# Performance work log

Measured on AMD Instinct MI355X. Metric: run time of the kernel, lower is better.

## Reference

```python
import jax, jax.numpy as jnp
import numpy as np

B, K, D, H, A = 8192, 10, 64, 128, 16
E = K * (K - 1)
# lexicographic ordered pairs (i,j), i != j -- matches adj.nonzero() and sorted(Dict.keys())
_PAIRS = np.array([(i, j) for i in range(K) for j in range(K) if i != j], dtype=np.int32)
SRC = jnp.asarray(_PAIRS[:, 0])  # message for edge (i,j) is aggregated at node i (row)
DST = jnp.asarray(_PAIRS[:, 1])


def setup_inputs() -> dict:
    key = jax.random.key(0)
    k1, k2, k3, k4, k5, k6 = jax.random.split(key, 6)
    F = D + H + A  # node MLP input dim
    return {
        "states": jax.random.normal(k1, (B, K, D), jnp.float32),
        "action_vec": jax.random.normal(k2, (B, K, A), jnp.float32),
        # one Linear(2D -> H) per ordered pair, stacked [E, 2D, H]
        "W_edge": jax.random.normal(k3, (E, 2 * D, H), jnp.float32) * (1.0 / np.sqrt(2 * D)),
        "b_edge": jax.random.normal(k4, (E, H), jnp.float32) * 0.01,
        # one Linear(D+H+A -> D) per node, stacked [K, F, D]
        "W_node": jax.random.normal(k5, (K, F, D), jnp.float32) * (1.0 / np.sqrt(F)),
        "b_node": jax.random.normal(k6, (K, D), jnp.float32) * 0.01,
    }


def reference(states, action_vec, W_edge, b_edge, W_node, b_node):
    # states: [B,K,D], action_vec: [B,K,A]
    b, k, d = states.shape
    # gather endpoints per ordered edge: [B,E,2D]
    pair_feat = jnp.concatenate([states[:, SRC, :], states[:, DST, :]], axis=-1)
    # per-edge-type Linear + tanh, batched as one grouped GEMM: [B,E,H]
    msg = jnp.tanh(jnp.einsum('bef,efh->beh', pair_feat, W_edge) + b_edge)
    # unsorted_segment_sum over source node index (row): [B,K,H]
    agg = jnp.zeros((b, k, msg.shape[-1]), msg.dtype).at[:, SRC, :].add(msg)
    # node input: [x, action, agg] -> per-node Linear + tanh: [B,K,D]
    node_in = jnp.concatenate([states, action_vec, agg], axis=-1)
    out = jnp.tanh(jnp.einsum('bkf,kfd->bkd', node_in, W_node) + b_node)
    return out
```

## Files before the change

### kernel.cpp

```cpp
#include <hip/hip_runtime.h>

typedef _Float16 f16;
typedef _Float16 f16x4 __attribute__((ext_vector_type(4)));
typedef _Float16 f16x8 __attribute__((ext_vector_type(8)));
typedef float    f32x4 __attribute__((ext_vector_type(4)));

#define S2C 2.88539008177792681472f

#define OFF_STF  0u
#define OFF_AC   5242880u
#define OFF_WEF  6553600u
#define OFF_WNF  8028160u
#define OFF_BE2  8171520u
#define OFF_Z    8195840u

__device__ __forceinline__ float fast_exp2(float x){
#if __has_builtin(__builtin_amdgcn_exp2f)
    return __builtin_amdgcn_exp2f(x);
#else
    return exp2f(x);
#endif
}
__device__ __forceinline__ float fast_rcp(float x){
#if __has_builtin(__builtin_amdgcn_rcpf)
    return __builtin_amdgcn_rcpf(x);
#else
    return 1.0f/x;
#endif
}

#define MFMA16(a,b,c) __builtin_amdgcn_mfma_f32_16x16x32_f16(a,b,c,0,0,0)

__global__ void prep(const float* __restrict__ st, const float* __restrict__ ac,
                     const float* __restrict__ We, const float* __restrict__ be,
                     const float* __restrict__ Wn, const float* __restrict__ bn,
                     f16* __restrict__ ws16){
    const int bid = blockIdx.x, t = threadIdx.x;
    if (bid < 2560){
        int g = bid*256 + t;
        int lane = g&63, ks = (g>>6)&1, rt = (g>>7)&1, rg2 = (g>>8)&255, node = g>>16;
        int row = rg2*32 + rt*16 + (lane&15);
        int k   = ks*32 + (lane>>4)*8;
        const float* src = st + ((size_t)row*10 + node)*64 + k;
        const float4 v0 = *(const float4*)src;
        const float4 v1 = *(const float4*)(src+4);
        f16x8 h; h[0]=(f16)v0.x; h[1]=(f16)v0.y; h[2]=(f16)v0.z; h[3]=(f16)v0.w;
                 h[4]=(f16)v1.x; h[5]=(f16)v1.y; h[6]=(f16)v1.z; h[7]=(f16)v1.w;
        *(f16x8*)(ws16 + OFF_STF + (size_t)g*8) = h;
    } else if (bid < 3840){
        int g = (bid-2560)*256 + t;
        const float4 v = ((const float4*)ac)[g];
        f16x4 h; h[0]=(f16)v.x; h[1]=(f16)v.y; h[2]=(f16)v.z; h[3]=(f16)v.w;
        *(f16x4*)(ws16 + OFF_AC + (size_t)g*4) = h;
    } else if (bid < 4560){
        int g = (bid-3840)*256 + t;
        int l = g & 15, q = (g>>4)&3, cg = (g>>6)&7, ks = (g>>9)&3, e = g>>11;
        const float* src = We + e*16384 + (ks*32 + q*8)*128 + cg*16 + l;
        f16x8 h;
        #pragma unroll
        for (int u=0;u<8;u++) h[u] = (f16)src[u*128];
        *(f16x8*)(ws16 + OFF_WEF + (size_t)g*8) = h;
    } else if (bid < 4630){
        int g = (bid-4560)*256 + t;
        if (g < 17920){
            int l = g&15, q=(g>>4)&3, c=(g>>6)&3, r=g>>8;
            int ks2 = r % 7, kn = r / 7;
            f16x8 h;
            #pragma unroll
            for (int u=0;u<8;u++){
                int knew = ks2*32 + q*8 + u;
                int f = (knew < 128) ? (knew + 80) : (knew - 128);
                h[u] = (knew < 208) ? (f16)Wn[kn*13312 + f*64 + c*16 + l] : (f16)0.0f;
            }
            *(f16x8*)(ws16 + OFF_WNF + (size_t)kn*14336 + ((size_t)(ks2*4+c)*64 + q*16 + l)*8) = h;
        }
    } else {
        int g = (bid-4630)*256 + t;
        float* be2 = (float*)(ws16 + OFF_BE2);
        if (g < 11520)      be2[g] = S2C*be[g];
        else if (g < 12160) be2[g] = S2C*bn[g-11520];
        else if (g < 12168) ws16[OFF_Z + (g-12160)] = (f16)0.0f;
    }
}

__launch_bounds__(256, 3)
__global__ void gnn_main(const f16* __restrict__ ws16, float* __restrict__ out){
    __shared__ alignas(16) f16 sAgg[64*128];

    const f16* stf = ws16 + OFF_STF;
    const f16* Wef = ws16 + OFF_WEF;
    const float* be2 = (const float*)(ws16 + OFF_BE2);
    const float* bn2 = be2 + 11520;

    const int t = threadIdx.x, lane = t&63, wid = t>>6;
    const int l15 = lane&15, q = lane>>4, qo = q<<3;
    const int i  = blockIdx.x >> 7;
    const int rb = blockIdx.x & 127;
    const int b0 = rb*64;
    const int rg2 = rb*2 + (wid>>1);
    const int cs  = wid&1;

    f16x8 ai[4];
    {
        const f16* p = stf + (size_t)(i*256 + rg2)*2048 + lane*8;
        ai[0] = *(const f16x8*)p;        ai[1] = *(const f16x8*)(p+512);
        ai[2] = *(const f16x8*)(p+1024); ai[3] = *(const f16x8*)(p+1536);
    }

    f32x4 agg[2][4] = {};

    #pragma unroll 1
    for (int e=0; e<9; ++e){
        const int j = e + (e >= i);
        const int ebase = 9*i + e;

        f16x8 aj[4];
        {
            const f16* p = stf + (size_t)(j*256 + rg2)*2048 + lane*8;
            aj[0] = *(const f16x8*)p;        aj[1] = *(const f16x8*)(p+512);
            aj[2] = *(const f16x8*)(p+1024); aj[3] = *(const f16x8*)(p+1536);
        }
        float bv[4];
        #pragma unroll
        for (int c=0; c<4; ++c) bv[c] = be2[ebase*128 + cs*64 + c*16 + l15];

        f32x4 msg[2][4] = {};
        #pragma unroll
        for (int ks4=0; ks4<4; ++ks4){
            const f16* wb = Wef + (size_t)((ebase*4 + ks4)*8 + cs*4)*512 + lane*8;
            f16x8 bf[4];
            #pragma unroll
            for (int c=0; c<4; ++c) bf[c] = *(const f16x8*)(wb + c*512);
            #pragma unroll
            for (int rt=0; rt<2; ++rt){
                f16x8 a = (ks4 < 2) ? ai[rt*2 + ks4] : aj[rt*2 + (ks4-2)];
                #pragma unroll
                for (int c=0; c<4; ++c)
                    msg[rt][c] = MFMA16(a, bf[c], msg[rt][c]);
            }
        }
        #pragma unroll
        for (int rt=0; rt<2; ++rt)
            #pragma unroll
            for (int c=0; c<4; ++c)
                #pragma unroll
                for (int r2=0; r2<4; ++r2){
                    float tt = __builtin_fmaf(msg[rt][c][r2], S2C, bv[c]);
                    float rr = fast_rcp(fast_exp2(tt) + 1.0f);
                    agg[rt][c][r2] = __builtin_fmaf(-2.0f, rr, agg[rt][c][r2]);
                }
    }

    #pragma unroll
    for (int rt=0; rt<2; ++rt)
        #pragma unroll
        for (int c=0; c<4; ++c)
            #pragma unroll
            for (int r2=0; r2<4; ++r2){
                int lrow = (wid>>1)*32 + rt*16 + q*4 + r2;
                int col  = cs*64 + c*16 + l15;
                sAgg[lrow*128 + (((col>>3) ^ (lrow&7))<<3) + (col&7)] = (f16)(agg[rt][c][r2] + 9.0f);
            }
    __syncthreads();

    f32x4 acc[4] = {};
    const f16* wnb = ws16 + OFF_WNF + (size_t)i*14336;
    const f16* acp = ws16 + OFF_AC;
    const f16* zb  = ws16 + OFF_Z;
    #pragma unroll
    for (int ks2=0; ks2<7; ++ks2){
        f16x8 a;
        if (ks2 < 4){
            int lrow = wid*16 + l15;
            a = *(const f16x8*)(sAgg + lrow*128 + (((ks2*4 + q) ^ (l15&7))<<3));
        } else if (ks2 < 6){
            int fi = ((i*256 + rb*2 + (wid>>1))*2 + (wid&1))*2 + (ks2-4);
            a = *(const f16x8*)(stf + (size_t)fi*512 + lane*8);
        } else {
            int row = b0 + wid*16 + l15;
            const f16* ap = (q < 2) ? (acp + ((size_t)row*10 + i)*16 + qo) : zb;
            a = *(const f16x8*)ap;
        }
        f16x8 bf[4];
        #pragma unroll
        for (int c=0; c<4; ++c)
            bf[c] = *(const f16x8*)(wnb + (size_t)(ks2*4+c)*512 + lane*8);
        #pragma unroll
        for (int c=0; c<4; ++c)
            acc[c] = MFMA16(a, bf[c], acc[c]);
    }
    float bnv[4];
    #pragma unroll
    for (int c=0; c<4; ++c) bnv[c] = bn2[i*64 + c*16 + l15];
    #pragma unroll
    for (int c=0; c<4; ++c)
        #pragma unroll
        for (int r2=0; r2<4; ++r2){
            int row = b0 + wid*16 + q*4 + r2;
            int col = c*16 + l15;
            float tt = __builtin_fmaf(acc[c][r2], S2C, bnv[c]);
            float rr = fast_rcp(fast_exp2(tt) + 1.0f);
            out[((size_t)row*10 + i)*64 + col] = __builtin_fmaf(-2.0f, rr, 1.0f);
        }
}

extern "C" void kernel_launch(void* const* d_in, const int* in_sizes, int n_in,
                              void* d_out, int out_size, void* d_ws, size_t ws_size,
                              hipStream_t stream) {
    const float* states = (const float*)d_in[0];
    const float* action = (const float*)d_in[1];
    const float* W_edge = (const float*)d_in[2];
    const float* b_edge = (const float*)d_in[3];
    const float* W_node = (const float*)d_in[4];
    const float* b_node = (const float*)d_in[5];
    f16* ws16 = (f16*)d_ws;

    hipLaunchKernelGGL(prep, dim3(4678), dim3(256), 0, stream,
                       states, action, W_edge, b_edge, W_node, b_node, ws16);
    hipLaunchKernelGGL(gnn_main, dim3(1280), dim3(256), 0, stream,
                       ws16, (float*)d_out);
}
```

Measured before the change: 156.4 us.

## Double-buffer edge weights in LDS via async global-to-LDS loads with larger blocks

Edge-weight tiles are now staged into LDS with global_load_lds and double-buffered, so the next edge's weights load while the current edge's MFMAs run. Blocks double to 512 threads covering 128 rows, so each weight tile is shared by 8 waves instead of 4. This cuts redundant global and L2 weight reads. In exchange it adds a block-wide barrier per edge iteration, uses 64KB of LDS per block, and halves the grid to 640 blocks, which may limit occupancy.

```diff
diff --git a/kernel.cpp b/kernel.cpp
--- a/kernel.cpp
+++ b/kernel.cpp
@@ -27,6 +27,12 @@
 #else
     return 1.0f/x;
 #endif
+}
+
+__device__ __forceinline__ void gl_lds16(const f16* g, f16* l){
+    __builtin_amdgcn_global_load_lds(
+        (const __attribute__((address_space(1))) unsigned int*)g,
+        (__attribute__((address_space(3))) unsigned int*)l, 16, 0, 0);
 }
 
 #define MFMA16(a,b,c) __builtin_amdgcn_mfma_f32_16x16x32_f16(a,b,c,0,0,0)
@@ -83,9 +89,9 @@
     }
 }
 
-__launch_bounds__(256, 3)
+__launch_bounds__(512, 4)
 __global__ void gnn_main(const f16* __restrict__ ws16, float* __restrict__ out){
-    __shared__ alignas(16) f16 sAgg[64*128];
+    __shared__ alignas(16) f16 S[32768];
 
     const f16* stf = ws16 + OFF_STF;
     const f16* Wef = ws16 + OFF_WEF;
@@ -94,26 +100,40 @@
 
     const int t = threadIdx.x, lane = t&63, wid = t>>6;
     const int l15 = lane&15, q = lane>>4, qo = q<<3;
-    const int i  = blockIdx.x >> 7;
-    const int rb = blockIdx.x & 127;
-    const int b0 = rb*64;
-    const int rg2 = rb*2 + (wid>>1);
-    const int cs  = wid&1;
-
+    const int rg = wid>>1, cs = wid&1;
+    const int i  = blockIdx.x >> 6;
+    const int rb = blockIdx.x & 63;
+    const int b0 = rb*128;
+    const int rg2 = rb*4 + rg;
+
+    const int e0 = 9*i;
+    {
+        const f16* wsrc = Wef + (size_t)e0*16384;
+        #pragma unroll
+        for (int it=0; it<4; ++it)
+            gl_lds16(wsrc + (wid*4+it)*512 + lane*8, S + (wid*4+it)*512);
+    }
     f16x8 ai[4];
     {
         const f16* p = stf + (size_t)(i*256 + rg2)*2048 + lane*8;
         ai[0] = *(const f16x8*)p;        ai[1] = *(const f16x8*)(p+512);
         ai[2] = *(const f16x8*)(p+1024); ai[3] = *(const f16x8*)(p+1536);
     }
-
     f32x4 agg[2][4] = {};
+    __syncthreads();
 
     #pragma unroll 1
     for (int e=0; e<9; ++e){
+        const int ebase = e0 + e;
         const int j = e + (e >= i);
-        const int ebase = 9*i + e;
-
+
+        if (e < 8){
+            const f16* wsrc = Wef + (size_t)(ebase+1)*16384;
+            f16* wdst = S + (((e+1)&1)<<14);
+            #pragma unroll
+            for (int it=0; it<4; ++it)
+                gl_lds16(wsrc + (wid*4+it)*512 + lane*8, wdst + (wid*4+it)*512);
+        }
         f16x8 aj[4];
         {
             const f16* p = stf + (size_t)(j*256 + rg2)*2048 + lane*8;
@@ -124,13 +144,13 @@
         #pragma unroll
         for (int c=0; c<4; ++c) bv[c] = be2[ebase*128 + cs*64 + c*16 + l15];
 
+        const f16* wb = S + ((e&1)<<14) + (size_t)(cs*4)*512 + lane*8;
         f32x4 msg[2][4] = {};
         #pragma unroll
         for (int ks4=0; ks4<4; ++ks4){
-            const f16* wb = Wef + (size_t)((ebase*4 + ks4)*8 + cs*4)*512 + lane*8;
             f16x8 bf[4];
             #pragma unroll
-            for (int c=0; c<4; ++c) bf[c] = *(const f16x8*)(wb + c*512);
+            for (int c=0; c<4; ++c) bf[c] = *(const f16x8*)(wb + (ks4*8 + c)*512);
             #pragma unroll
             for (int rt=0; rt<2; ++rt){
                 f16x8 a = (ks4 < 2) ? ai[rt*2 + ks4] : aj[rt*2 + (ks4-2)];
@@ -149,6 +169,7 @@
                     float rr = fast_rcp(fast_exp2(tt) + 1.0f);
                     agg[rt][c][r2] = __builtin_fmaf(-2.0f, rr, agg[rt][c][r2]);
                 }
+        __syncthreads();
     }
 
     #pragma unroll
@@ -157,9 +178,9 @@
         for (int c=0; c<4; ++c)
             #pragma unroll
             for (int r2=0; r2<4; ++r2){
-                int lrow = (wid>>1)*32 + rt*16 + q*4 + r2;
+                int lrow = rg*32 + rt*16 + q*4 + r2;
                 int col  = cs*64 + c*16 + l15;
-                sAgg[lrow*128 + (((col>>3) ^ (lrow&7))<<3) + (col&7)] = (f16)(agg[rt][c][r2] + 9.0f);
+                S[lrow*128 + (((col>>3) ^ (lrow&7))<<3) + (col&7)] = (f16)(agg[rt][c][r2] + 9.0f);
             }
     __syncthreads();
 
@@ -172,9 +193,9 @@
         f16x8 a;
         if (ks2 < 4){
             int lrow = wid*16 + l15;
-            a = *(const f16x8*)(sAgg + lrow*128 + (((ks2*4 + q) ^ (l15&7))<<3));
+            a = *(const f16x8*)(S + lrow*128 + (((ks2*4 + q) ^ (l15&7))<<3));
         } else if (ks2 < 6){
-            int fi = ((i*256 + rb*2 + (wid>>1))*2 + (wid&1))*2 + (ks2-4);
+            int fi = ((i*256 + rb*4 + (wid>>1))*2 + (wid&1))*2 + (ks2-4);
             a = *(const f16x8*)(stf + (size_t)fi*512 + lane*8);
         } else {
             int row = b0 + wid*16 + l15;
@@ -217,6 +238,6 @@
 
     hipLaunchKernelGGL(prep, dim3(4678), dim3(256), 0, stream,
                        states, action, W_edge, b_edge, W_node, b_node, ws16);
-    hipLaunchKernelGGL(gnn_main, dim3(1280), dim3(256), 0, stream,
+    hipLaunchKernelGGL(gnn_main, dim3(640), dim3(512), 0, stream,
                        ws16, (float*)d_out);
 }
```

Result: faster. 141.5 us (-9.6%).
